# Performance work log

Hardware: AMD Instinct MI355X
Metric: run time of the kernel (lower is better)

The kernel has to match this reference:

```python
import jax, jax.numpy as jnp
import numpy as np

N_LEVELS = 16
FPL = 2                      # n_features_per_level
LOG2_T = 19
T = 1 << LOG2_T              # hashmap size per level
BASE_RES = 16
MAX_RES = 4096
NEURONS = 64
N_PTS = 524288
AABB_MIN, AABB_MAX = -1.0, 1.0

_b = np.exp((np.log(MAX_RES) - np.log(BASE_RES)) / (N_LEVELS - 1))
RES = jnp.asarray(np.floor(BASE_RES * _b ** np.arange(N_LEVELS)).astype(np.float32))  # [L]
PRIMES = jnp.array([1, 2654435761, 805459861], dtype=jnp.uint32)
OFFS = jnp.array([[(i >> d) & 1 for d in range(3)] for i in range(8)], dtype=jnp.uint32)  # [8,3]


def hash_encode(x, table):
    # x: [N,3] in [0,1], table: [L, T, FPL]
    N = x.shape[0]
    scaled = x[:, None, :] * RES[None, :, None]          # [N,L,3]
    pos = jnp.floor(scaled)
    w = scaled - pos                                      # trilinear frac weights [N,L,3]
    corner = pos.astype(jnp.uint32)[:, :, None, :] + OFFS[None, None]   # [N,L,8,3]
    h = corner * PRIMES                                   # uint32 wrap-around mult
    idx = (h[..., 0] ^ h[..., 1] ^ h[..., 2]) & jnp.uint32(T - 1)       # [N,L,8]
    flat_idx = (idx + (jnp.arange(N_LEVELS, dtype=jnp.uint32) * T)[None, :, None]).astype(jnp.int32)
    emb = table.reshape(N_LEVELS * T, FPL)[flat_idx]      # [N,L,8,FPL] gather
    offf = OFFS.astype(x.dtype)[None, None]               # [1,1,8,3]
    wc = jnp.prod(jnp.where(offf > 0, w[:, :, None, :], 1.0 - w[:, :, None, :]), axis=-1)  # [N,L,8]
    feat = jnp.sum(emb * wc[..., None], axis=2)           # [N,L,FPL]
    return feat.reshape(N, N_LEVELS * FPL)


def setup_inputs() -> dict:
    key = jax.random.key(0)
    ks = jax.random.split(key, 6)
    positions = jax.random.uniform(ks[0], (N_PTS, 3), minval=-1.0, maxval=1.0)
    table = jax.random.uniform(ks[1], (N_LEVELS, T, FPL), minval=-1e-4, maxval=1e-4)
    in_dim = N_LEVELS * FPL
    def w(k, m, n):
        return jax.random.normal(k, (m, n), dtype=jnp.float32) * float(1.0 / np.sqrt(m))
    W0 = w(ks[2], in_dim, NEURONS)
    W1 = w(ks[3], NEURONS, NEURONS)
    W2 = w(ks[4], NEURONS, NEURONS)
    W3 = w(ks[5], NEURONS, 4)
    return {"positions": positions, "table": table, "W0": W0, "W1": W1, "W2": W2, "W3": W3}


def reference(positions, table, W0, W1, W2, W3):
    x = (positions - AABB_MIN) / (AABB_MAX - AABB_MIN)            # normalize into [0,1]
    selector = jnp.all((x > 0.0) & (x < 1.0), axis=-1)            # [N]
    feat = hash_encode(x, table)                                  # [N, L*FPL]
    h = jax.nn.relu(feat @ W0)
    h = jax.nn.relu(h @ W1)
    h = jax.nn.relu(h @ W2)
    out = h @ W3                                                  # [N,4]
    rgb = jax.nn.sigmoid(out[:, :3])
    density = jnp.exp(out[:, 3:4] - 1.0) * selector[:, None].astype(out.dtype)  # trunc_exp(x-1)
    return rgb, density
```

## Files before the change

kernel.cpp:

```cpp
#include <hip/hip_runtime.h>
#include <hip/hip_bf16.h>

#define NLEV 16
#define TSIZE (1u << 19)
#define TMASK ((1u << 19) - 1u)
#define P1 2654435761u
#define P2 805459861u
#define FP8_SCALE 8192.0f
#define FP8_INV (1.0f / 8192.0f)

typedef __attribute__((ext_vector_type(8))) short short8;
typedef __attribute__((ext_vector_type(4))) float f32x4;

__device__ __constant__ float c_res[NLEV] = {
    16.f, 23.f, 33.f, 48.f, 70.f, 101.f, 147.f, 212.f,
    307.f, 445.f, 645.f, 933.f, 1351.f, 1955.f, 2830.f, 4096.f};

__device__ __forceinline__ short bf16_bits(float v) {
    __hip_bfloat16 h = __float2bfloat16(v);
    unsigned short us;
    __builtin_memcpy(&us, &h, 2);
    return (short)us;
}

__device__ __forceinline__ unsigned pack2_bf16(float lo, float hi) {
    unsigned a = (unsigned short)bf16_bits(lo);
    unsigned b = (unsigned short)bf16_bits(hi);
    return a | (b << 16);
}

__global__ __launch_bounds__(256) void convert_table_fp8_kernel(
    const float2* __restrict__ table, unsigned* __restrict__ pq, int total)
{
    for (int i = blockIdx.x * 256 + threadIdx.x; i < total; i += gridDim.x * 256) {
        float2 e = table[i];
        float nx = __shfl_xor(e.x, 1);
        float ny = __shfl_xor(e.y, 1);
        unsigned lo = __builtin_amdgcn_cvt_pk_fp8_f32(e.x * FP8_SCALE, e.y * FP8_SCALE, 0u, false);
        unsigned all4 = __builtin_amdgcn_cvt_pk_fp8_f32(nx * FP8_SCALE, ny * FP8_SCALE, lo, true);
        pq[i] = all4;
    }
}

__global__ __launch_bounds__(256) void hash_encode_fp8_kernel(
    const float* __restrict__ pos,
    const unsigned* __restrict__ pq,
    __hip_bfloat162* __restrict__ feat,
    int n, unsigned nb4)
{
    unsigned b = blockIdx.x;
    unsigned slot = b & 7u;
    unsigned jj = b >> 3u;
    unsigned l = slot + 8u * (jj / nb4);
    unsigned pblk = jj % nb4;
    const int tid = threadIdx.x;
    const float r = c_res[l];
    const unsigned* tl = pq + (size_t)l * TSIZE;

    unsigned gq[16];
    float wxl[4], wyl[4], wzl[4];
    unsigned sll[4];
    int idx[4];

#pragma unroll
    for (int k = 0; k < 4; ++k) {
        int i = (int)(pblk * 1024u) + 256 * k + tid;
        if (i >= n) i = n - 1;
        idx[k] = i;
        float x = (pos[3 * i + 0] + 1.f) * 0.5f;
        float y = (pos[3 * i + 1] + 1.f) * 0.5f;
        float z = (pos[3 * i + 2] + 1.f) * 0.5f;
        float sx = x * r, sy = y * r, sz = z * r;
        float fx = floorf(sx), fy = floorf(sy), fz = floorf(sz);
        wxl[k] = sx - fx; wyl[k] = sy - fy; wzl[k] = sz - fz;
        unsigned ix = (unsigned)fx, iy = (unsigned)fy, iz = (unsigned)fz;
        unsigned hy0 = iy * P1, hy1 = hy0 + P1;
        unsigned hz0 = iz * P2, hz1 = hz0 + P2;
        unsigned a00 = hy0 ^ hz0, a10 = hy1 ^ hz0;
        unsigned a01 = hy0 ^ hz1, a11 = hy1 ^ hz1;
        unsigned sel = ix & 1u;
        unsigned jx = ix + sel;
        sll[k] = sel;
        gq[4 * k + 0] = tl[(jx ^ a00) & TMASK];
        gq[4 * k + 1] = tl[(jx ^ a10) & TMASK];
        gq[4 * k + 2] = tl[(jx ^ a01) & TMASK];
        gq[4 * k + 3] = tl[(jx ^ a11) & TMASK];
    }

#pragma unroll
    for (int k = 0; k < 4; ++k) {
        float wx = wxl[k], wy = wyl[k], wz = wzl[k];
        bool s = sll[k] != 0u;
        unsigned u00 = gq[4 * k + 0], u10 = gq[4 * k + 1];
        unsigned u01 = gq[4 * k + 2], u11 = gq[4 * k + 3];

        float a0_00 = __builtin_amdgcn_cvt_f32_fp8(u00, 0), a1_00 = __builtin_amdgcn_cvt_f32_fp8(u00, 1);
        float b0_00 = __builtin_amdgcn_cvt_f32_fp8(u00, 2), b1_00 = __builtin_amdgcn_cvt_f32_fp8(u00, 3);
        float a0_10 = __builtin_amdgcn_cvt_f32_fp8(u10, 0), a1_10 = __builtin_amdgcn_cvt_f32_fp8(u10, 1);
        float b0_10 = __builtin_amdgcn_cvt_f32_fp8(u10, 2), b1_10 = __builtin_amdgcn_cvt_f32_fp8(u10, 3);
        float a0_01 = __builtin_amdgcn_cvt_f32_fp8(u01, 0), a1_01 = __builtin_amdgcn_cvt_f32_fp8(u01, 1);
        float b0_01 = __builtin_amdgcn_cvt_f32_fp8(u01, 2), b1_01 = __builtin_amdgcn_cvt_f32_fp8(u01, 3);
        float a0_11 = __builtin_amdgcn_cvt_f32_fp8(u11, 0), a1_11 = __builtin_amdgcn_cvt_f32_fp8(u11, 1);
        float b0_11 = __builtin_amdgcn_cvt_f32_fp8(u11, 2), b1_11 = __builtin_amdgcn_cvt_f32_fp8(u11, 3);

        float lo0_00 = s ? b0_00 : a0_00, hi0_00 = s ? a0_00 : b0_00;
        float lo1_00 = s ? b1_00 : a1_00, hi1_00 = s ? a1_00 : b1_00;
        float lo0_10 = s ? b0_10 : a0_10, hi0_10 = s ? a0_10 : b0_10;
        float lo1_10 = s ? b1_10 : a1_10, hi1_10 = s ? a1_10 : b1_10;
        float lo0_01 = s ? b0_01 : a0_01, hi0_01 = s ? a0_01 : b0_01;
        float lo1_01 = s ? b1_01 : a1_01, hi1_01 = s ? a1_01 : b1_01;
        float lo0_11 = s ? b0_11 : a0_11, hi0_11 = s ? a0_11 : b0_11;
        float lo1_11 = s ? b1_11 : a1_11, hi1_11 = s ? a1_11 : b1_11;

        float ux = 1.f - wx, uy = 1.f - wy, uz = 1.f - wz;
        float w000 = ux * uy * uz, w100 = wx * uy * uz;
        float w010 = ux * wy * uz, w110 = wx * wy * uz;
        float w001 = ux * uy * wz, w101 = wx * uy * wz;
        float w011 = ux * wy * wz, w111 = wx * wy * wz;

        float f0 = lo0_00 * w000 + hi0_00 * w100 + lo0_10 * w010 + hi0_10 * w110 +
                   lo0_01 * w001 + hi0_01 * w101 + lo0_11 * w011 + hi0_11 * w111;
        float f1 = lo1_00 * w000 + hi1_00 * w100 + lo1_10 * w010 + hi1_10 * w110 +
                   lo1_01 * w001 + hi1_01 * w101 + lo1_11 * w011 + hi1_11 * w111;

        __hip_bfloat162 v;
        v.x = __float2bfloat16(f0 * FP8_INV);
        v.y = __float2bfloat16(f1 * FP8_INV);
        feat[(size_t)l * n + idx[k]] = v;
    }
}

__global__ __launch_bounds__(256) void hash_encode_kernel(
    const float* __restrict__ pos,
    const float* __restrict__ table,
    __hip_bfloat162* __restrict__ feat,
    int n, unsigned bpl)
{
    unsigned b = blockIdx.x;
    unsigned slot = b & 7u;
    unsigned jj = b >> 3u;
    unsigned l = slot + 8u * (jj / bpl);
    unsigned pblk = jj % bpl;
    int i = (int)(pblk * 256u + threadIdx.x);
    if (i >= n) return;

    float x = (pos[3 * i + 0] + 1.f) * 0.5f;
    float y = (pos[3 * i + 1] + 1.f) * 0.5f;
    float z = (pos[3 * i + 2] + 1.f) * 0.5f;

    float r = c_res[l];
    float sx = x * r, sy = y * r, sz = z * r;
    float fx = floorf(sx), fy = floorf(sy), fz = floorf(sz);
    float wx = sx - fx, wy = sy - fy, wz = sz - fz;
    unsigned ix = (unsigned)fx, iy = (unsigned)fy, iz = (unsigned)fz;
    unsigned hy0 = iy * P1, hy1 = hy0 + P1;
    unsigned hz0 = iz * P2, hz1 = hz0 + P2;
    unsigned a00 = hy0 ^ hz0, a10 = hy1 ^ hz0;
    unsigned a01 = hy0 ^ hz1, a11 = hy1 ^ hz1;
    unsigned ix1 = ix + 1u;

    const float2* tl = (const float2*)table + (size_t)l * TSIZE;
    float2 e000 = tl[(ix  ^ a00) & TMASK];
    float2 e100 = tl[(ix1 ^ a00) & TMASK];
    float2 e010 = tl[(ix  ^ a10) & TMASK];
    float2 e110 = tl[(ix1 ^ a10) & TMASK];
    float2 e001 = tl[(ix  ^ a01) & TMASK];
    float2 e101 = tl[(ix1 ^ a01) & TMASK];
    float2 e011 = tl[(ix  ^ a11) & TMASK];
    float2 e111 = tl[(ix1 ^ a11) & TMASK];

    float ux = 1.f - wx, uy = 1.f - wy, uz = 1.f - wz;
    float w000 = ux * uy * uz, w100 = wx * uy * uz;
    float w010 = ux * wy * uz, w110 = wx * wy * uz;
    float w001 = ux * uy * wz, w101 = wx * uy * wz;
    float w011 = ux * wy * wz, w111 = wx * wy * wz;

    float f0 = e000.x * w000 + e100.x * w100 + e010.x * w010 + e110.x * w110 +
               e001.x * w001 + e101.x * w101 + e011.x * w011 + e111.x * w111;
    float f1 = e000.y * w000 + e100.y * w100 + e010.y * w010 + e110.y * w110 +
               e001.y * w001 + e101.y * w101 + e011.y * w011 + e111.y * w111;

    __hip_bfloat162 v;
    v.x = __float2bfloat16(f0);
    v.y = __float2bfloat16(f1);
    feat[(size_t)l * n + i] = v;
}

__device__ __forceinline__ void store_H(char* hrow, int g, int swz, f32x4* acc) {
#pragma unroll
    for (int mt = 0; mt < 4; ++mt) {
        float v0 = fmaxf(acc[mt][0], 0.f), v1 = fmaxf(acc[mt][1], 0.f);
        float v2 = fmaxf(acc[mt][2], 0.f), v3 = fmaxf(acc[mt][3], 0.f);
        unsigned lo = pack2_bf16(v0, v1);
        unsigned hi = pack2_bf16(v2, v3);
        int blk = (2 * mt + (g >> 1)) ^ swz;
        *(uint2*)(hrow + blk * 16 + (g & 1) * 8) = make_uint2(lo, hi);
    }
}

__global__ __launch_bounds__(256) void mlp_mfma_kernel(
    const float* __restrict__ pos,
    const unsigned* __restrict__ feat,
    const float* __restrict__ W0,
    const float* __restrict__ W1,
    const float* __restrict__ W2,
    const float* __restrict__ W3,
    float* __restrict__ out, int n, int nchunks)
{
    __shared__ char hlds[4 * 16 * 128];
    const int tid  = threadIdx.x;
    const int w    = tid >> 6;
    const int lane = tid & 63;
    const int g    = lane >> 4;
    const int p    = lane & 15;
    char* hrow = hlds + w * (16 * 128) + p * 128;
    const int swz = p & 7;

    short8 a0[4], a1[4][2], a2[4][2], a3[2];
#pragma unroll
    for (int mt = 0; mt < 4; ++mt)
#pragma unroll
        for (int jj = 0; jj < 8; ++jj)
            a0[mt][jj] = bf16_bits(W0[(8 * g + jj) * 64 + 16 * mt + p]);
#pragma unroll
    for (int mt = 0; mt < 4; ++mt)
#pragma unroll
        for (int kt = 0; kt < 2; ++kt)
#pragma unroll
            for (int jj = 0; jj < 8; ++jj) {
                a1[mt][kt][jj] = bf16_bits(W1[(32 * kt + 8 * g + jj) * 64 + 16 * mt + p]);
                a2[mt][kt][jj] = bf16_bits(W2[(32 * kt + 8 * g + jj) * 64 + 16 * mt + p]);
            }
#pragma unroll
    for (int kt = 0; kt < 2; ++kt)
#pragma unroll
        for (int jj = 0; jj < 8; ++jj)
            a3[kt][jj] = (p < 4) ? bf16_bits(W3[(32 * kt + 8 * g + jj) * 4 + p]) : (short)0;

    const f32x4 zf = {0.f, 0.f, 0.f, 0.f};

    for (int c = blockIdx.x; c < nchunks; c += gridDim.x) {
        const int base = c * 256 + w * 64;
        for (int t = 0; t < 4; ++t) {
            const int ptg = base + t * 16 + p;
            const int ptc = ptg < n ? ptg : n - 1;

            union { unsigned u[4]; short8 s; } bu;
#pragma unroll
            for (int m = 0; m < 4; ++m)
                bu.u[m] = feat[(size_t)(4 * g + m) * (size_t)n + ptc];

            f32x4 acc[4];
#pragma unroll
            for (int mt = 0; mt < 4; ++mt)
                acc[mt] = __builtin_amdgcn_mfma_f32_16x16x32_bf16(a0[mt], bu.s, zf, 0, 0, 0);

            store_H(hrow, g, swz, acc);
            short8 b0 = *(const short8*)(hrow + ((g ^ swz) << 4));
            short8 b1 = *(const short8*)(hrow + (((4 + g) ^ swz) << 4));

#pragma unroll
            for (int mt = 0; mt < 4; ++mt) {
                acc[mt] = __builtin_amdgcn_mfma_f32_16x16x32_bf16(a1[mt][0], b0, zf, 0, 0, 0);
                acc[mt] = __builtin_amdgcn_mfma_f32_16x16x32_bf16(a1[mt][1], b1, acc[mt], 0, 0, 0);
            }

            store_H(hrow, g, swz, acc);
            b0 = *(const short8*)(hrow + ((g ^ swz) << 4));
            b1 = *(const short8*)(hrow + (((4 + g) ^ swz) << 4));

#pragma unroll
            for (int mt = 0; mt < 4; ++mt) {
                acc[mt] = __builtin_amdgcn_mfma_f32_16x16x32_bf16(a2[mt][0], b0, zf, 0, 0, 0);
                acc[mt] = __builtin_amdgcn_mfma_f32_16x16x32_bf16(a2[mt][1], b1, acc[mt], 0, 0, 0);
            }

            store_H(hrow, g, swz, acc);
            b0 = *(const short8*)(hrow + ((g ^ swz) << 4));
            b1 = *(const short8*)(hrow + (((4 + g) ^ swz) << 4));

            f32x4 o = __builtin_amdgcn_mfma_f32_16x16x32_bf16(a3[0], b0, zf, 0, 0, 0);
            o = __builtin_amdgcn_mfma_f32_16x16x32_bf16(a3[1], b1, o, 0, 0, 0);

            if (g == 0 && ptg < n) {
                float px = pos[3 * ptg + 0];
                float py = pos[3 * ptg + 1];
                float pz = pos[3 * ptg + 2];
                float xx = (px + 1.f) * 0.5f;
                float yy = (py + 1.f) * 0.5f;
                float zz = (pz + 1.f) * 0.5f;
                bool sel = (xx > 0.f) && (xx < 1.f) && (yy > 0.f) && (yy < 1.f) &&
                           (zz > 0.f) && (zz < 1.f);
                out[3 * (size_t)ptg + 0] = 1.f / (1.f + expf(-o[0]));
                out[3 * (size_t)ptg + 1] = 1.f / (1.f + expf(-o[1]));
                out[3 * (size_t)ptg + 2] = 1.f / (1.f + expf(-o[2]));
                out[3 * (size_t)n + ptg] = expf(o[3] - 1.f) * (sel ? 1.f : 0.f);
            }
        }
    }
}

__global__ __launch_bounds__(256) void hashgrid_fused_kernel(
    const float* __restrict__ pos, const float* __restrict__ table,
    const float* __restrict__ W0, const float* __restrict__ W1,
    const float* __restrict__ W2, const float* __restrict__ W3,
    float* __restrict__ out, int n)
{
    int id = blockIdx.x * 256 + threadIdx.x;
    int i = id < n ? id : n - 1;

    float x = (pos[3 * i + 0] + 1.f) * 0.5f;
    float y = (pos[3 * i + 1] + 1.f) * 0.5f;
    float z = (pos[3 * i + 2] + 1.f) * 0.5f;
    bool sel = (x > 0.f) && (x < 1.f) && (y > 0.f) && (y < 1.f) &&
               (z > 0.f) && (z < 1.f);

    float h0[64];
#pragma unroll
    for (int j = 0; j < 64; ++j) h0[j] = 0.f;

    const float2* tb = (const float2*)table;
#pragma unroll
    for (int l = 0; l < NLEV; ++l) {
        float r = c_res[l];
        float sx = x * r, sy = y * r, sz = z * r;
        float fx = floorf(sx), fy = floorf(sy), fz = floorf(sz);
        float wx = sx - fx, wy = sy - fy, wz = sz - fz;
        unsigned ix = (unsigned)fx, iy = (unsigned)fy, iz = (unsigned)fz;
        unsigned hy0 = iy * P1, hy1 = hy0 + P1;
        unsigned hz0 = iz * P2, hz1 = hz0 + P2;
        unsigned a00 = hy0 ^ hz0, a10 = hy1 ^ hz0;
        unsigned a01 = hy0 ^ hz1, a11 = hy1 ^ hz1;
        unsigned ix1 = ix + 1u;
        const float2* tl = tb + (size_t)l * TSIZE;
        float2 e000 = tl[(ix  ^ a00) & TMASK];
        float2 e100 = tl[(ix1 ^ a00) & TMASK];
        float2 e010 = tl[(ix  ^ a10) & TMASK];
        float2 e110 = tl[(ix1 ^ a10) & TMASK];
        float2 e001 = tl[(ix  ^ a01) & TMASK];
        float2 e101 = tl[(ix1 ^ a01) & TMASK];
        float2 e011 = tl[(ix  ^ a11) & TMASK];
        float2 e111 = tl[(ix1 ^ a11) & TMASK];

        float ux = 1.f - wx, uy = 1.f - wy, uz = 1.f - wz;
        float w000 = ux * uy * uz, w100 = wx * uy * uz;
        float w010 = ux * wy * uz, w110 = wx * wy * uz;
        float w001 = ux * uy * wz, w101 = wx * uy * wz;
        float w011 = ux * wy * wz, w111 = wx * wy * wz;

        float f0 = e000.x * w000 + e100.x * w100 + e010.x * w010 + e110.x * w110 +
                   e001.x * w001 + e101.x * w101 + e011.x * w011 + e111.x * w111;
        float f1 = e000.y * w000 + e100.y * w100 + e010.y * w010 + e110.y * w110 +
                   e001.y * w001 + e101.y * w101 + e011.y * w011 + e111.y * w111;

        const float* w0a = W0 + (2 * l) * 64;
        const float* w0b = W0 + (2 * l + 1) * 64;
#pragma unroll
        for (int j = 0; j < 64; ++j)
            h0[j] = fmaf(f0, w0a[j], fmaf(f1, w0b[j], h0[j]));
    }
#pragma unroll
    for (int j = 0; j < 64; ++j) h0[j] = fmaxf(h0[j], 0.f);

    float h1[64];
#pragma unroll
    for (int j = 0; j < 64; ++j) h1[j] = 0.f;
#pragma unroll
    for (int k = 0; k < 64; ++k) {
        float v = h0[k];
        const float* wr = W1 + k * 64;
#pragma unroll
        for (int j = 0; j < 64; ++j) h1[j] = fmaf(v, wr[j], h1[j]);
    }
#pragma unroll
    for (int j = 0; j < 64; ++j) h1[j] = fmaxf(h1[j], 0.f);

#pragma unroll
    for (int j = 0; j < 64; ++j) h0[j] = 0.f;
#pragma unroll
    for (int k = 0; k < 64; ++k) {
        float v = h1[k];
        const float* wr = W2 + k * 64;
#pragma unroll
        for (int j = 0; j < 64; ++j) h0[j] = fmaf(v, wr[j], h0[j]);
    }
#pragma unroll
    for (int j = 0; j < 64; ++j) h0[j] = fmaxf(h0[j], 0.f);

    float o0 = 0.f, o1 = 0.f, o2 = 0.f, o3 = 0.f;
#pragma unroll
    for (int k = 0; k < 64; ++k) {
        float v = h0[k];
        const float* wr = W3 + k * 4;
        o0 = fmaf(v, wr[0], o0);
        o1 = fmaf(v, wr[1], o1);
        o2 = fmaf(v, wr[2], o2);
        o3 = fmaf(v, wr[3], o3);
    }

    if (id < n) {
        float r = 1.f / (1.f + expf(-o0));
        float g = 1.f / (1.f + expf(-o1));
        float b = 1.f / (1.f + expf(-o2));
        float d = expf(o3 - 1.f) * (sel ? 1.f : 0.f);
        out[3 * (size_t)i + 0] = r;
        out[3 * (size_t)i + 1] = g;
        out[3 * (size_t)i + 2] = b;
        out[3 * (size_t)n + i] = d;
    }
}

extern "C" void kernel_launch(void* const* d_in, const int* in_sizes, int n_in,
                              void* d_out, int out_size, void* d_ws, size_t ws_size,
                              hipStream_t stream) {
    const float* pos   = (const float*)d_in[0];
    const float* table = (const float*)d_in[1];
    const float* W0    = (const float*)d_in[2];
    const float* W1    = (const float*)d_in[3];
    const float* W2    = (const float*)d_in[4];
    const float* W3    = (const float*)d_in[5];
    float* out = (float*)d_out;
    int n = in_sizes[0] / 3;
    unsigned bpl = (unsigned)((n + 255) / 256);
    unsigned nb4 = (unsigned)((n + 1023) / 1024);
    int nchunks = (n + 255) / 256;
    int mblocks = nchunks < 512 ? nchunks : 512;

    size_t pq_bytes   = (size_t)NLEV * TSIZE * sizeof(unsigned);
    size_t feat_bytes = (size_t)NLEV * n * sizeof(__hip_bfloat162);

    if (ws_size >= pq_bytes + feat_bytes) {
        unsigned* pq = (unsigned*)d_ws;
        __hip_bfloat162* feat = (__hip_bfloat162*)((char*)d_ws + pq_bytes);
        int total = NLEV * (int)TSIZE;
        hipLaunchKernelGGL(convert_table_fp8_kernel, dim3(2048), dim3(256), 0, stream,
                           (const float2*)table, pq, total);
        hipLaunchKernelGGL(hash_encode_fp8_kernel, dim3(16 * nb4), dim3(256), 0, stream,
                           pos, pq, feat, n, nb4);
        hipLaunchKernelGGL(mlp_mfma_kernel, dim3(mblocks), dim3(256), 0, stream,
                           pos, (const unsigned*)feat, W0, W1, W2, W3, out, n, nchunks);
    } else if (ws_size >= feat_bytes) {
        __hip_bfloat162* feat = (__hip_bfloat162*)d_ws;
        hipLaunchKernelGGL(hash_encode_kernel, dim3(16 * bpl), dim3(256), 0, stream,
                           pos, table, feat, n, bpl);
        hipLaunchKernelGGL(mlp_mfma_kernel, dim3(mblocks), dim3(256), 0, stream,
                           pos, (const unsigned*)feat, W0, W1, W2, W3, out, n, nchunks);
    } else {
        hipLaunchKernelGGL(hashgrid_fused_kernel, dim3(bpl), dim3(256), 0, stream,
                           pos, table, W0, W1, W2, W3, out, n);
    }
}
```

Before: 190.6 us.

## Add dense per-cell corner tables for coarse levels, split fine-level hash work

For the four coarsest levels, a new kernel builds a dense grid where each cell stores all 8 corner features as FP8 in one uint4. A second new kernel then interpolates each point from that single 16-byte load instead of eight scattered hash gathers. The FP8 table conversion now covers only levels 4-15, and the hash kernel remaps its blocks to those 12 levels with each level split into two point halves. The MLP grid cap also rises from 512 to 2048 blocks. The cost is extra kernel launches and building the dense tables on every call.

```diff
diff --git a/kernel.cpp b/kernel.cpp
--- a/kernel.cpp
+++ b/kernel.cpp
@@ -9,12 +9,18 @@
 #define FP8_SCALE 8192.0f
 #define FP8_INV (1.0f / 8192.0f)
 
+#define NDENSE 4
+#define DTOTAL 189332
+
 typedef __attribute__((ext_vector_type(8))) short short8;
 typedef __attribute__((ext_vector_type(4))) float f32x4;
 
 __device__ __constant__ float c_res[NLEV] = {
     16.f, 23.f, 33.f, 48.f, 70.f, 101.f, 147.f, 212.f,
     307.f, 445.f, 645.f, 933.f, 1351.f, 1955.f, 2830.f, 4096.f};
+
+__device__ __constant__ int c_cdim[NDENSE] = {18, 25, 35, 50};
+__device__ __constant__ int c_doff[NDENSE] = {0, 5832, 21457, 64332};
 
 __device__ __forceinline__ short bf16_bits(float v) {
     __hip_bfloat16 h = __float2bfloat16(v);
@@ -30,32 +36,120 @@
 }
 
 __global__ __launch_bounds__(256) void convert_table_fp8_kernel(
-    const float2* __restrict__ table, unsigned* __restrict__ pq, int total)
+    const float2* __restrict__ table, unsigned* __restrict__ pq,
+    int start, int total)
 {
     for (int i = blockIdx.x * 256 + threadIdx.x; i < total; i += gridDim.x * 256) {
-        float2 e = table[i];
+        int ig = start + i;
+        float2 e = table[ig];
         float nx = __shfl_xor(e.x, 1);
         float ny = __shfl_xor(e.y, 1);
         unsigned lo = __builtin_amdgcn_cvt_pk_fp8_f32(e.x * FP8_SCALE, e.y * FP8_SCALE, 0u, false);
         unsigned all4 = __builtin_amdgcn_cvt_pk_fp8_f32(nx * FP8_SCALE, ny * FP8_SCALE, lo, true);
-        pq[i] = all4;
-    }
+        pq[ig] = all4;
+    }
+}
+
+__global__ __launch_bounds__(256) void build_dense_kernel(
+    const float2* __restrict__ table, uint4* __restrict__ dense)
+{
+    int t = blockIdx.x * 256 + threadIdx.x;
+    if (t >= DTOTAL) return;
+    int l = 3;
+    if (t < c_doff[1]) l = 0;
+    else if (t < c_doff[2]) l = 1;
+    else if (t < c_doff[3]) l = 2;
+    int rel = t - c_doff[l];
+    int dim = c_cdim[l];
+    int ix = rel % dim;
+    int rem = rel / dim;
+    int iy = rem % dim;
+    int iz = rem / dim;
+    const float2* tl = table + (size_t)l * TSIZE;
+
+    float2 v[8];
+#pragma unroll
+    for (int e = 0; e < 8; ++e) {
+        unsigned cx = (unsigned)(ix + (e & 1));
+        unsigned cy = (unsigned)(iy + ((e >> 1) & 1));
+        unsigned cz = (unsigned)(iz + (e >> 2));
+        unsigned h = (cx ^ (cy * P1) ^ (cz * P2)) & TMASK;
+        v[e] = tl[h];
+    }
+    unsigned w[4];
+#pragma unroll
+    for (int d = 0; d < 4; ++d) {
+        unsigned lo = __builtin_amdgcn_cvt_pk_fp8_f32(v[2 * d].x * FP8_SCALE,
+                                                      v[2 * d].y * FP8_SCALE, 0u, false);
+        w[d] = __builtin_amdgcn_cvt_pk_fp8_f32(v[2 * d + 1].x * FP8_SCALE,
+                                               v[2 * d + 1].y * FP8_SCALE, lo, true);
+    }
+    dense[t] = make_uint4(w[0], w[1], w[2], w[3]);
+}
+
+__global__ __launch_bounds__(256) void dense_lookup_kernel(
+    const float* __restrict__ pos, const uint4* __restrict__ dense,
+    __hip_bfloat162* __restrict__ feat, int n)
+{
+    int i = blockIdx.x * 256 + threadIdx.x;
+    int l = blockIdx.y;
+    if (i >= n) return;
+
+    float x = (pos[3 * i + 0] + 1.f) * 0.5f;
+    float y = (pos[3 * i + 1] + 1.f) * 0.5f;
+    float z = (pos[3 * i + 2] + 1.f) * 0.5f;
+    float r = c_res[l];
+    float sx = x * r, sy = y * r, sz = z * r;
+    float fx = floorf(sx), fy = floorf(sy), fz = floorf(sz);
+    float wx = sx - fx, wy = sy - fy, wz = sz - fz;
+    int dim = c_cdim[l];
+    unsigned ix = (unsigned)fx, iy = (unsigned)fy, iz = (unsigned)fz;
+    ix = ix > (unsigned)(dim - 2) ? (unsigned)(dim - 2) : ix;
+    iy = iy > (unsigned)(dim - 2) ? (unsigned)(dim - 2) : iy;
+    iz = iz > (unsigned)(dim - 2) ? (unsigned)(dim - 2) : iz;
+
+    uint4 wv = dense[(size_t)c_doff[l] + ((size_t)iz * dim + iy) * dim + ix];
+    unsigned dw[4] = {wv.x, wv.y, wv.z, wv.w};
+
+    float ux = 1.f - wx, uy = 1.f - wy, uz = 1.f - wz;
+    float wyz[4] = {uy * uz, wy * uz, uy * wz, wy * wz};
+
+    float f0 = 0.f, f1 = 0.f;
+#pragma unroll
+    for (int d = 0; d < 4; ++d) {
+        unsigned word = dw[d];
+        float we = ux * wyz[d];
+        float wo = wx * wyz[d];
+        f0 += __builtin_amdgcn_cvt_f32_fp8(word, 0) * we
+            + __builtin_amdgcn_cvt_f32_fp8(word, 2) * wo;
+        f1 += __builtin_amdgcn_cvt_f32_fp8(word, 1) * we
+            + __builtin_amdgcn_cvt_f32_fp8(word, 3) * wo;
+    }
+
+    __hip_bfloat162 v;
+    v.x = __float2bfloat16(f0 * FP8_INV);
+    v.y = __float2bfloat16(f1 * FP8_INV);
+    feat[(size_t)l * n + i] = v;
 }
 
 __global__ __launch_bounds__(256) void hash_encode_fp8_kernel(
     const float* __restrict__ pos,
     const unsigned* __restrict__ pq,
     __hip_bfloat162* __restrict__ feat,
-    int n, unsigned nb4)
+    int n, unsigned halfn, unsigned nbh)
 {
     unsigned b = blockIdx.x;
     unsigned slot = b & 7u;
     unsigned jj = b >> 3u;
-    unsigned l = slot + 8u * (jj / nb4);
-    unsigned pblk = jj % nb4;
+    unsigned ur = jj / nbh;
+    unsigned pb = jj % nbh;
+    unsigned u = slot + 8u * ur;
+    unsigned l = 4u + (u >> 1);
+    unsigned half = u & 1u;
     const int tid = threadIdx.x;
     const float r = c_res[l];
     const unsigned* tl = pq + (size_t)l * TSIZE;
+    const int base = (int)(half * halfn + pb * 1024u);
 
     unsigned gq[16];
     float wxl[4], wyl[4], wzl[4];
@@ -64,7 +158,7 @@
 
 #pragma unroll
     for (int k = 0; k < 4; ++k) {
-        int i = (int)(pblk * 1024u) + 256 * k + tid;
+        int i = base + 256 * k + tid;
         if (i >= n) i = n - 1;
         idx[k] = i;
         float x = (pos[3 * i + 0] + 1.f) * 0.5f;
@@ -422,21 +516,28 @@
     float* out = (float*)d_out;
     int n = in_sizes[0] / 3;
     unsigned bpl = (unsigned)((n + 255) / 256);
-    unsigned nb4 = (unsigned)((n + 1023) / 1024);
+    unsigned halfn = (unsigned)((n + 1) / 2);
+    unsigned nbh = (halfn + 1023) / 1024;
     int nchunks = (n + 255) / 256;
-    int mblocks = nchunks < 512 ? nchunks : 512;
-
-    size_t pq_bytes   = (size_t)NLEV * TSIZE * sizeof(unsigned);
-    size_t feat_bytes = (size_t)NLEV * n * sizeof(__hip_bfloat162);
-
-    if (ws_size >= pq_bytes + feat_bytes) {
+    int mblocks = nchunks < 2048 ? nchunks : 2048;
+
+    size_t pq_bytes    = (size_t)NLEV * TSIZE * sizeof(unsigned);
+    size_t dense_bytes = (size_t)DTOTAL * sizeof(uint4);
+    size_t feat_bytes  = (size_t)NLEV * n * sizeof(__hip_bfloat162);
+
+    if (ws_size >= pq_bytes + dense_bytes + feat_bytes) {
         unsigned* pq = (unsigned*)d_ws;
-        __hip_bfloat162* feat = (__hip_bfloat162*)((char*)d_ws + pq_bytes);
-        int total = NLEV * (int)TSIZE;
+        uint4* dense = (uint4*)((char*)d_ws + pq_bytes);
+        __hip_bfloat162* feat = (__hip_bfloat162*)((char*)d_ws + pq_bytes + dense_bytes);
+
+        hipLaunchKernelGGL(build_dense_kernel, dim3((DTOTAL + 255) / 256), dim3(256),
+                           0, stream, (const float2*)table, dense);
         hipLaunchKernelGGL(convert_table_fp8_kernel, dim3(2048), dim3(256), 0, stream,
-                           (const float2*)table, pq, total);
-        hipLaunchKernelGGL(hash_encode_fp8_kernel, dim3(16 * nb4), dim3(256), 0, stream,
-                           pos, pq, feat, n, nb4);
+                           (const float2*)table, pq, 4 * (int)TSIZE, 12 * (int)TSIZE);
+        hipLaunchKernelGGL(dense_lookup_kernel, dim3(bpl, NDENSE), dim3(256), 0, stream,
+                           pos, dense, feat, n);
+        hipLaunchKernelGGL(hash_encode_fp8_kernel, dim3(24 * nbh), dim3(256), 0, stream,
+                           pos, pq, feat, n, halfn, nbh);
         hipLaunchKernelGGL(mlp_mfma_kernel, dim3(mblocks), dim3(256), 0, stream,
                            pos, (const unsigned*)feat, W0, W1, W2, W3, out, n, nchunks);
     } else if (ws_size >= feat_bytes) {
```

New measurement: 182.1 us. -4.5%, faster.
